# Optimization experiments

Hardware: AMD Instinct MI355X
Metric: run time of the kernel (lower is better)

The kernel has to match this reference:

```python
import jax, jax.numpy as jnp
import numpy as np

B1, B2 = 4096, 4096
DF, MF = 1024, 512
H1, H2, H3, H1_ = 2048, 1024, 512, 1024
DO, MO = 1, 1


def _lin(x, W, b):
    return x @ W.T + b


def setup_inputs() -> dict:
    key = jax.random.key(0)
    ks = jax.random.split(key, 22)

    def w(k, o, i):
        return (jax.random.normal(k, (o, i), jnp.float32) / np.sqrt(i)).astype(jnp.float32)

    def bz(k, o):
        return jax.random.normal(k, (o,), jnp.float32) * 0.01

    return {
        'x1': jax.random.normal(ks[0], (B1, DF), jnp.float32),
        'x2': jax.random.normal(ks[1], (B2, MF), jnp.float32),
        'W1_1': w(ks[2], H1, DF),  'b1_1': bz(ks[3], H1),
        'W1_2': w(ks[4], H2, H1),  'b1_2': bz(ks[5], H2),
        'W1_3': w(ks[6], H3, H2),  'b1_3': bz(ks[7], H3),
        'W1_4': w(ks[8], H2, H3),  'b1_4': bz(ks[9], H2),
        'W1_5': w(ks[10], H1, H2), 'b1_5': bz(ks[11], H1),
        'Wp1':  w(ks[12], DO, H1), 'bp1':  bz(ks[13], DO),
        'W2_1': w(ks[14], H1_, MF), 'b2_1': bz(ks[15], H1_),
        'W2_2': w(ks[16], H3, H1_), 'b2_2': bz(ks[17], H3),
        'W2_3': w(ks[18], H1_, H3), 'b2_3': bz(ks[19], H1_),
        'Wp2':  w(ks[20], MO, H1_), 'bp2':  bz(ks[21], MO),
    }


def reference(x1, x2, W1_1, b1_1, W1_2, b1_2, W1_3, b1_3, W1_4, b1_4,
              W1_5, b1_5, Wp1, bp1, W2_1, b2_1, W2_2, b2_2, W2_3, b2_3,
              Wp2, bp2):
    # dropout: eval mode (identity)
    h = jax.nn.relu(_lin(x1, W1_1, b1_1))
    h = jax.nn.relu(_lin(h, W1_2, b1_2))
    x_1 = jax.nn.sigmoid(_lin(h, W1_3, b1_3))          # [B1, H3]
    h = jax.nn.relu(_lin(x_1, W1_4, b1_4))
    h = jax.nn.relu(_lin(h, W1_5, b1_5))
    x2_1 = jax.nn.sigmoid(_lin(h, Wp1, bp1))           # [B1, DO]

    g = jax.nn.relu(_lin(x2, W2_1, b2_1))
    x_2 = jax.nn.sigmoid(_lin(g, W2_2, b2_2))          # [B2, H3]
    g = jax.nn.relu(_lin(x_2, W2_3, b2_3))
    x2_2 = jax.nn.sigmoid(_lin(g, Wp2, bp2))           # [B2, MO]

    # Python loop over x_1 rows doing (x_2 * row).sum(1) == single GEMM x_1 @ x_2.T
    scores = x_1 @ x_2.T                                # [B1, B2]
    pre_dm = scores.reshape(-1)                         # row-major matches torch.cat order
    # MinMaxScaler.fit_transform on detached values (original uses .data -> no grad)
    pre_dm = jax.lax.stop_gradient(pre_dm)
    mn, mx = pre_dm.min(), pre_dm.max()
    pre_dm = (pre_dm - mn) / (mx - mn)

    pre_data = x2_1.reshape(-1)
    pre_model = x2_2.T.reshape(-1)
    return (pre_data, pre_dm, pre_model)
```

## Files before the change

### kernel.cpp

```cpp
#include <hip/hip_runtime.h>
#include <hip/hip_bf16.h>

typedef __bf16 bf16_t;
typedef bf16_t bf16x8 __attribute__((ext_vector_type(8)));
typedef bf16_t bf16x4 __attribute__((ext_vector_type(4)));
typedef float f32x4 __attribute__((ext_vector_type(4)));

typedef __attribute__((address_space(1))) const void gconst_void;
typedef __attribute__((address_space(3))) void lds_void;

__device__ __forceinline__ void async16(const bf16_t* g, bf16_t* l) {
  __builtin_amdgcn_global_load_lds((gconst_void*)g, (lds_void*)l, 16, 0, 0);
}

#define WAIT_VM4() __builtin_amdgcn_s_waitcnt(0xF74)
#define WAIT_VM0() __builtin_amdgcn_s_waitcnt(0xF70)

struct CvtDesc { const float* src; bf16_t* dst; long n; };
struct CvtArgs { CvtDesc d[10]; };

__global__ __launch_bounds__(256) void cvt_many(CvtArgs a) {
  const CvtDesc de = a.d[blockIdx.y];
  long i = ((long)blockIdx.x * 256 + threadIdx.x) * 4;
  const long stride = (long)gridDim.x * 256 * 4;
  for (; i < de.n; i += stride) {
    float4 v = *(const float4*)(de.src + i);
    bf16x4 o;
    o[0] = (bf16_t)v.x; o[1] = (bf16_t)v.y; o[2] = (bf16_t)v.z; o[3] = (bf16_t)v.w;
    *(bf16x4*)(de.dst + i) = o;
  }
}

struct GDesc {
  const bf16_t* A; const bf16_t* W; const float* bias; void* C;
  int N, K, act;
};
struct GArgs { GDesc d[2]; int ntiles0; };

template <typename OutT, bool MINMAX>
__global__ __launch_bounds__(256) void gemm_gb(GArgs ga, float* __restrict__ pmin,
                                               float* __restrict__ pmax) {
  const int b = blockIdx.x;
  const int p = (b >= ga.ntiles0) ? 1 : 0;
  const GDesc d = ga.d[p];
  const int local = b - (p ? ga.ntiles0 : 0);
  const int bm = (local & 31) * 128;
  const int bn = (local >> 5) * 128;
  const int N = d.N, K = d.K;
  const int NK = K >> 5;

  const int SB = 128 * 32;
  __shared__ __align__(16) bf16_t As[3 * 128 * 32];
  __shared__ __align__(16) bf16_t Bs[3 * 128 * 32];

  const int t = threadIdx.x;
  const int wave = t >> 6;
  const int lane = t & 63;
  const int quad = lane >> 4;
  const int l15 = lane & 15;
  const int wm = (wave >> 1) * 64;
  const int wn = (wave & 1) * 64;

  f32x4 acc[4][4];
#pragma unroll
  for (int i = 0; i < 4; ++i)
#pragma unroll
    for (int j = 0; j < 4; ++j) acc[i][j] = (f32x4){0.f, 0.f, 0.f, 0.f};

  const int c0 = t, c1 = t + 256;
  const int r0 = c0 >> 2, kc0 = ((c0 & 3) - r0) & 3;
  const int r1 = c1 >> 2, kc1 = ((c1 & 3) - r1) & 3;
  const bf16_t* pa0 = d.A + (long)(bm + r0) * K + kc0 * 8;
  const bf16_t* pa1 = d.A + (long)(bm + r1) * K + kc1 * 8;
  const bf16_t* pw0 = d.W + (long)(bn + r0) * K + kc0 * 8;
  const bf16_t* pw1 = d.W + (long)(bn + r1) * K + kc1 * 8;
  bf16_t* lA0 = &As[c0 * 8]; bf16_t* lA1 = &As[c1 * 8];
  bf16_t* lB0 = &Bs[c0 * 8]; bf16_t* lB1 = &Bs[c1 * 8];

  async16(pa0, lA0);            async16(pa1, lA1);
  async16(pw0, lB0);            async16(pw1, lB1);
  async16(pa0 + 32, lA0 + SB);  async16(pa1 + 32, lA1 + SB);
  async16(pw0 + 32, lB0 + SB);  async16(pw1 + 32, lB1 + SB);

  int cs = 0;
  int ps = 2 * SB;
  for (int k = 0; k < NK; ++k) {
    if (k < NK - 1) WAIT_VM4(); else WAIT_VM0();
    __builtin_amdgcn_s_barrier();
    if (k + 2 < NK) {
      const int ko = (k + 2) * 32;
      async16(pa0 + ko, lA0 + ps); async16(pa1 + ko, lA1 + ps);
      async16(pw0 + ko, lB0 + ps); async16(pw1 + ko, lB1 + ps);
    }
    const bf16_t* as = As + cs;
    const bf16_t* bs = Bs + cs;
    bf16x8 af[4], bfr[4];
#pragma unroll
    for (int i = 0; i < 4; ++i) {
      const int r = wm + i * 16 + l15;
      af[i] = *(const bf16x8*)&as[r * 32 + ((quad + r) & 3) * 8];
    }
#pragma unroll
    for (int j = 0; j < 4; ++j) {
      const int r = wn + j * 16 + l15;
      bfr[j] = *(const bf16x8*)&bs[r * 32 + ((quad + r) & 3) * 8];
    }
#pragma unroll
    for (int i = 0; i < 4; ++i)
#pragma unroll
      for (int j = 0; j < 4; ++j)
        acc[i][j] = __builtin_amdgcn_mfma_f32_16x16x32_bf16(af[i], bfr[j],
                                                            acc[i][j], 0, 0, 0);
    cs += SB; if (cs == 3 * SB) cs = 0;
    ps += SB; if (ps == 3 * SB) ps = 0;
  }

  OutT* C = (OutT*)d.C;
  const int row0 = bm + wm + quad * 4;
  const int col0 = bn + wn + l15;
  float mn = 3.4e38f, mx = -3.4e38f;
#pragma unroll
  for (int j = 0; j < 4; ++j) {
    const int col = col0 + j * 16;
    const float bv = d.bias ? d.bias[col] : 0.f;
#pragma unroll
    for (int i = 0; i < 4; ++i) {
#pragma unroll
      for (int r = 0; r < 4; ++r) {
        float v = acc[i][j][r] + bv;
        if (d.act == 1) v = fmaxf(v, 0.f);
        else if (d.act == 2) v = 1.f / (1.f + expf(-v));
        C[(long)(row0 + i * 16 + r) * N + col] = (OutT)v;
        if (MINMAX) { mn = fminf(mn, v); mx = fmaxf(mx, v); }
      }
    }
  }
  if (MINMAX) {
#pragma unroll
    for (int off = 32; off > 0; off >>= 1) {
      mn = fminf(mn, __shfl_down(mn, off));
      mx = fmaxf(mx, __shfl_down(mx, off));
    }
    __shared__ float smn[4], smx[4];
    if (lane == 0) { smn[wave] = mn; smx[wave] = mx; }
    __syncthreads();
    if (t == 0) {
      pmin[blockIdx.x] = fminf(fminf(smn[0], smn[1]), fminf(smn[2], smn[3]));
      pmax[blockIdx.x] = fmaxf(fmaxf(smx[0], smx[1]), fmaxf(smx[2], smx[3]));
    }
  }
}

struct RDesc { const bf16_t* A; const float* w; const float* b; float* out; int K; };

__global__ __launch_bounds__(64) void rowdot2(RDesc d0, RDesc d1) {
  const RDesc d = blockIdx.y ? d1 : d0;
  const int row = blockIdx.x;
  const int lane = threadIdx.x;
  const bf16_t* a = d.A + (long)row * d.K;
  float s = 0.f;
  for (int k = lane * 8; k < d.K; k += 64 * 8) {
    bf16x8 av = *(const bf16x8*)&a[k];
    float4 w0 = *(const float4*)&d.w[k];
    float4 w1 = *(const float4*)&d.w[k + 4];
    s += (float)av[0] * w0.x + (float)av[1] * w0.y +
         (float)av[2] * w0.z + (float)av[3] * w0.w +
         (float)av[4] * w1.x + (float)av[5] * w1.y +
         (float)av[6] * w1.z + (float)av[7] * w1.w;
  }
#pragma unroll
  for (int off = 32; off > 0; off >>= 1) s += __shfl_down(s, off);
  if (lane == 0) d.out[row] = 1.f / (1.f + expf(-(s + d.b[0])));
}

__global__ __launch_bounds__(256) void minmax_final(
    const float* __restrict__ pmin, const float* __restrict__ pmax, int nb,
    float* __restrict__ res) {
  float mn = 3.4e38f, mx = -3.4e38f;
  for (int i = threadIdx.x; i < nb; i += 256) {
    mn = fminf(mn, pmin[i]);
    mx = fmaxf(mx, pmax[i]);
  }
#pragma unroll
  for (int off = 32; off > 0; off >>= 1) {
    mn = fminf(mn, __shfl_down(mn, off));
    mx = fmaxf(mx, __shfl_down(mx, off));
  }
  __shared__ float smn[4], smx[4];
  const int wv = threadIdx.x >> 6, ln = threadIdx.x & 63;
  if (ln == 0) { smn[wv] = mn; smx[wv] = mx; }
  __syncthreads();
  if (threadIdx.x == 0) {
    float m0 = fminf(fminf(smn[0], smn[1]), fminf(smn[2], smn[3]));
    float m1 = fmaxf(fmaxf(smx[0], smx[1]), fmaxf(smx[2], smx[3]));
    res[0] = m0;
    res[1] = 1.f / (m1 - m0);
  }
}

__global__ __launch_bounds__(256) void normalize_k(
    float* __restrict__ out, const float* __restrict__ res, long n) {
  const float mn = res[0], inv = res[1];
  long i = ((long)blockIdx.x * 256 + threadIdx.x) * 4;
  const long stride = (long)gridDim.x * 256 * 4;
  for (; i < n; i += stride) {
    float4 v = *(const float4*)&out[i];
    v.x = (v.x - mn) * inv;
    v.y = (v.y - mn) * inv;
    v.z = (v.z - mn) * inv;
    v.w = (v.w - mn) * inv;
    *(float4*)&out[i] = v;
  }
}

extern "C" void kernel_launch(void* const* d_in, const int* in_sizes, int n_in,
                              void* d_out, int out_size, void* d_ws,
                              size_t ws_size, hipStream_t stream) {
  const float* x1   = (const float*)d_in[0];
  const float* x2   = (const float*)d_in[1];
  const float* W1_1 = (const float*)d_in[2];   const float* b1_1 = (const float*)d_in[3];
  const float* W1_2 = (const float*)d_in[4];   const float* b1_2 = (const float*)d_in[5];
  const float* W1_3 = (const float*)d_in[6];   const float* b1_3 = (const float*)d_in[7];
  const float* W1_4 = (const float*)d_in[8];   const float* b1_4 = (const float*)d_in[9];
  const float* W1_5 = (const float*)d_in[10];  const float* b1_5 = (const float*)d_in[11];
  const float* Wp1  = (const float*)d_in[12];  const float* bp1  = (const float*)d_in[13];
  const float* W2_1 = (const float*)d_in[14];  const float* b2_1 = (const float*)d_in[15];
  const float* W2_2 = (const float*)d_in[16];  const float* b2_2 = (const float*)d_in[17];
  const float* W2_3 = (const float*)d_in[18];  const float* b2_3 = (const float*)d_in[19];
  const float* Wp2  = (const float*)d_in[20];  const float* bp2  = (const float*)d_in[21];

  float* out = (float*)d_out;
  float* out_pre_data  = out;
  float* out_pre_dm    = out + 4096;
  float* out_pre_model = out + 4096 + (long)4096 * 4096;

  char* arena = (char*)out_pre_dm;
  const size_t MB = 1024 * 1024;
  bf16_t* x1b   = (bf16_t*)(arena);
  bf16_t* x2b   = (bf16_t*)(arena + 8 * MB);
  bf16_t* W1_1b = (bf16_t*)(arena + 12 * MB);
  bf16_t* W1_2b = (bf16_t*)(arena + 16 * MB);
  bf16_t* W1_3b = (bf16_t*)(arena + 20 * MB);
  bf16_t* W1_4b = (bf16_t*)(arena + 21 * MB);
  bf16_t* W1_5b = (bf16_t*)(arena + 22 * MB);
  bf16_t* W2_1b = (bf16_t*)(arena + 26 * MB);
  bf16_t* W2_2b = (bf16_t*)(arena + 27 * MB);
  bf16_t* W2_3b = (bf16_t*)(arena + 28 * MB);
  bf16_t* bufA  = (bf16_t*)(arena + 32 * MB);
  bf16_t* bufB  = (bf16_t*)(arena + 48 * MB);
  bf16_t* bufC  = (bf16_t*)(arena + 56 * MB);

  char* ws = (char*)d_ws;
  bf16_t* bufX1 = (bf16_t*)(ws);
  bf16_t* bufX2 = (bf16_t*)(ws + 4 * MB);
  float* pmin = (float*)(ws + 8 * MB);
  float* pmax = pmin + 1024;
  float* res  = pmax + 1024;

  CvtArgs ca;
  ca.d[0] = {x1,   x1b,   (long)4096 * 1024};
  ca.d[1] = {x2,   x2b,   (long)4096 * 512};
  ca.d[2] = {W1_1, W1_1b, (long)2048 * 1024};
  ca.d[3] = {W1_2, W1_2b, (long)1024 * 2048};
  ca.d[4] = {W1_3, W1_3b, (long)512 * 1024};
  ca.d[5] = {W1_4, W1_4b, (long)1024 * 512};
  ca.d[6] = {W1_5, W1_5b, (long)2048 * 1024};
  ca.d[7] = {W2_1, W2_1b, (long)1024 * 512};
  ca.d[8] = {W2_2, W2_2b, (long)512 * 1024};
  ca.d[9] = {W2_3, W2_3b, (long)1024 * 512};
  cvt_many<<<dim3(192, 10), 256, 0, stream>>>(ca);

  const long nS = (long)4096 * 4096;
  GArgs g;

  g.d[0] = {x1b, W1_1b, b1_1, bufA, 2048, 1024, 1};
  g.d[1] = {x2b, W2_1b, b2_1, bufC, 1024, 512, 1};
  g.ntiles0 = 512;
  gemm_gb<bf16_t, false><<<768, 256, 0, stream>>>(g, nullptr, nullptr);

  g.d[0] = {bufA, W1_2b, b1_2, bufB, 1024, 2048, 1};
  g.d[1] = {bufC, W2_2b, b2_2, bufX2, 512, 1024, 2};
  g.ntiles0 = 256;
  gemm_gb<bf16_t, false><<<384, 256, 0, stream>>>(g, nullptr, nullptr);

  g.d[0] = {bufB, W1_3b, b1_3, bufX1, 512, 1024, 2};
  g.d[1] = {bufX2, W2_3b, b2_3, bufC, 1024, 512, 1};
  g.ntiles0 = 128;
  gemm_gb<bf16_t, false><<<384, 256, 0, stream>>>(g, nullptr, nullptr);

  g.d[0] = {bufX1, W1_4b, b1_4, bufB, 1024, 512, 1};
  g.d[1] = g.d[0];
  g.ntiles0 = 256;
  gemm_gb<bf16_t, false><<<256, 256, 0, stream>>>(g, nullptr, nullptr);

  g.d[0] = {bufB, W1_5b, b1_5, bufA, 2048, 1024, 1};
  g.d[1] = g.d[0];
  g.ntiles0 = 512;
  gemm_gb<bf16_t, false><<<512, 256, 0, stream>>>(g, nullptr, nullptr);

  RDesc r0 = {bufA, Wp1, bp1, out_pre_data, 2048};
  RDesc r1 = {bufC, Wp2, bp2, out_pre_model, 1024};
  rowdot2<<<dim3(4096, 2), 64, 0, stream>>>(r0, r1);

  g.d[0] = {bufX1, bufX2, nullptr, out_pre_dm, 4096, 512, 0};
  g.d[1] = g.d[0];
  g.ntiles0 = 1024;
  gemm_gb<float, true><<<1024, 256, 0, stream>>>(g, pmin, pmax);

  minmax_final<<<1, 256, 0, stream>>>(pmin, pmax, 1024, res);
  normalize_k<<<2048, 256, 0, stream>>>(out_pre_dm, res, nS);
}
```

Before: 364.7 us.

## Replace async global-to-LDS loads with register-staged double-buffered padded LDS tiles

Swaps the three-stage global_load_lds pipeline for a two-deep register prefetch. Each step writes the staged registers into a double-buffered LDS tile whose rows are padded to 40 elements, which replaces the XOR-style swizzle as the bank-conflict fix. The intent is more control over load and compute overlap and simpler LDS addressing. In exchange it uses more VGPRs for the staging registers, issues extra LDS store instructions, and waits only on LDS counters before the barrier, so correctness relies on compiler-inserted vmcnt waits for the global loads.

```diff
diff --git a/kernel.cpp b/kernel.cpp
--- a/kernel.cpp
+++ b/kernel.cpp
@@ -6,15 +6,7 @@
 typedef bf16_t bf16x4 __attribute__((ext_vector_type(4)));
 typedef float f32x4 __attribute__((ext_vector_type(4)));
 
-typedef __attribute__((address_space(1))) const void gconst_void;
-typedef __attribute__((address_space(3))) void lds_void;
-
-__device__ __forceinline__ void async16(const bf16_t* g, bf16_t* l) {
-  __builtin_amdgcn_global_load_lds((gconst_void*)g, (lds_void*)l, 16, 0, 0);
-}
-
-#define WAIT_VM4() __builtin_amdgcn_s_waitcnt(0xF74)
-#define WAIT_VM0() __builtin_amdgcn_s_waitcnt(0xF70)
+#define WAIT_LGKM0() __builtin_amdgcn_s_waitcnt(0xC07F)
 
 struct CvtDesc { const float* src; bf16_t* dst; long n; };
 struct CvtArgs { CvtDesc d[10]; };
@@ -36,6 +28,8 @@
   int N, K, act;
 };
 struct GArgs { GDesc d[2]; int ntiles0; };
+
+#define LDP 40
 
 template <typename OutT, bool MINMAX>
 __global__ __launch_bounds__(256) void gemm_gb(GArgs ga, float* __restrict__ pmin,
@@ -49,9 +43,8 @@
   const int N = d.N, K = d.K;
   const int NK = K >> 5;
 
-  const int SB = 128 * 32;
-  __shared__ __align__(16) bf16_t As[3 * 128 * 32];
-  __shared__ __align__(16) bf16_t Bs[3 * 128 * 32];
+  __shared__ __align__(16) bf16_t As[2][128 * LDP];
+  __shared__ __align__(16) bf16_t Bs[2][128 * LDP];
 
   const int t = threadIdx.x;
   const int wave = t >> 6;
@@ -68,51 +61,56 @@
     for (int j = 0; j < 4; ++j) acc[i][j] = (f32x4){0.f, 0.f, 0.f, 0.f};
 
   const int c0 = t, c1 = t + 256;
-  const int r0 = c0 >> 2, kc0 = ((c0 & 3) - r0) & 3;
-  const int r1 = c1 >> 2, kc1 = ((c1 & 3) - r1) & 3;
+  const int r0 = c0 >> 2, kc0 = c0 & 3;
+  const int r1 = c1 >> 2, kc1 = c1 & 3;
   const bf16_t* pa0 = d.A + (long)(bm + r0) * K + kc0 * 8;
   const bf16_t* pa1 = d.A + (long)(bm + r1) * K + kc1 * 8;
   const bf16_t* pw0 = d.W + (long)(bn + r0) * K + kc0 * 8;
   const bf16_t* pw1 = d.W + (long)(bn + r1) * K + kc1 * 8;
-  bf16_t* lA0 = &As[c0 * 8]; bf16_t* lA1 = &As[c1 * 8];
-  bf16_t* lB0 = &Bs[c0 * 8]; bf16_t* lB1 = &Bs[c1 * 8];
-
-  async16(pa0, lA0);            async16(pa1, lA1);
-  async16(pw0, lB0);            async16(pw1, lB1);
-  async16(pa0 + 32, lA0 + SB);  async16(pa1 + 32, lA1 + SB);
-  async16(pw0 + 32, lB0 + SB);  async16(pw1 + 32, lB1 + SB);
-
-  int cs = 0;
-  int ps = 2 * SB;
+  const int wa0 = r0 * LDP + kc0 * 8;
+  const int wa1 = r1 * LDP + kc1 * 8;
+
+  uint4 sA0[2], sA1[2], sB0[2], sB1[2];
+  sA0[0] = *(const uint4*)(pa0);       sA1[0] = *(const uint4*)(pa1);
+  sB0[0] = *(const uint4*)(pw0);       sB1[0] = *(const uint4*)(pw1);
+  sA0[1] = *(const uint4*)(pa0 + 32);  sA1[1] = *(const uint4*)(pa1 + 32);
+  sB0[1] = *(const uint4*)(pw0 + 32);  sB1[1] = *(const uint4*)(pw1 + 32);
+  *(uint4*)&As[0][wa0] = sA0[0];  *(uint4*)&As[0][wa1] = sA1[0];
+  *(uint4*)&Bs[0][wa0] = sB0[0];  *(uint4*)&Bs[0][wa1] = sB1[0];
+  WAIT_LGKM0();
+  __builtin_amdgcn_s_barrier();
+
   for (int k = 0; k < NK; ++k) {
-    if (k < NK - 1) WAIT_VM4(); else WAIT_VM0();
-    __builtin_amdgcn_s_barrier();
+    const int cur = k & 1;
     if (k + 2 < NK) {
       const int ko = (k + 2) * 32;
-      async16(pa0 + ko, lA0 + ps); async16(pa1 + ko, lA1 + ps);
-      async16(pw0 + ko, lB0 + ps); async16(pw1 + ko, lB1 + ps);
-    }
-    const bf16_t* as = As + cs;
-    const bf16_t* bs = Bs + cs;
+      const int st = k & 1;
+      sA0[st] = *(const uint4*)(pa0 + ko);  sA1[st] = *(const uint4*)(pa1 + ko);
+      sB0[st] = *(const uint4*)(pw0 + ko);  sB1[st] = *(const uint4*)(pw1 + ko);
+    }
+    const bf16_t* as = As[cur];
+    const bf16_t* bs = Bs[cur];
     bf16x8 af[4], bfr[4];
 #pragma unroll
-    for (int i = 0; i < 4; ++i) {
-      const int r = wm + i * 16 + l15;
-      af[i] = *(const bf16x8*)&as[r * 32 + ((quad + r) & 3) * 8];
-    }
-#pragma unroll
-    for (int j = 0; j < 4; ++j) {
-      const int r = wn + j * 16 + l15;
-      bfr[j] = *(const bf16x8*)&bs[r * 32 + ((quad + r) & 3) * 8];
-    }
+    for (int i = 0; i < 4; ++i)
+      af[i] = *(const bf16x8*)&as[(wm + i * 16 + l15) * LDP + quad * 8];
+#pragma unroll
+    for (int j = 0; j < 4; ++j)
+      bfr[j] = *(const bf16x8*)&bs[(wn + j * 16 + l15) * LDP + quad * 8];
 #pragma unroll
     for (int i = 0; i < 4; ++i)
 #pragma unroll
       for (int j = 0; j < 4; ++j)
         acc[i][j] = __builtin_amdgcn_mfma_f32_16x16x32_bf16(af[i], bfr[j],
                                                             acc[i][j], 0, 0, 0);
-    cs += SB; if (cs == 3 * SB) cs = 0;
-    ps += SB; if (ps == 3 * SB) ps = 0;
+    if (k + 1 < NK) {
+      const int nb = (k + 1) & 1;
+      const int ss = (k + 1) & 1;
+      *(uint4*)&As[nb][wa0] = sA0[ss];  *(uint4*)&As[nb][wa1] = sA1[ss];
+      *(uint4*)&Bs[nb][wa0] = sB0[ss];  *(uint4*)&Bs[nb][wa1] = sB1[ss];
+      WAIT_LGKM0();
+      __builtin_amdgcn_s_barrier();
+    }
   }
 
   OutT* C = (OutT*)d.C;
```

Measured after the change: 651.8 us. 1.79x slower.
